# Kernel tuning notes

Hardware: AMD Instinct MI355X
Metric: run time of the kernel (lower is better)

Reference implementation:

```python
import jax, jax.numpy as jnp
import numpy as np

N_CHANNEL = 64
N_BAND = 5
N_CLASS = 2
B = 64
K = 2 * N_CHANNEL  # nodes covered by the fully-connected edge_index


def _w(key, shape):
    fan_in = shape[0] if len(shape) == 2 else int(np.prod(shape[1:]))
    return (jax.random.normal(key, shape, jnp.float32) / np.float32(np.sqrt(fan_in)))


def setup_inputs() -> dict:
    key = jax.random.key(0)
    ks = jax.random.split(key, 22)
    d = {}
    d['x1'] = jax.random.normal(ks[0], (B, K, N_BAND), jnp.float32)
    d['x2'] = jax.random.normal(ks[1], (B, K, K), jnp.float32)
    # GCNConv params (weights stored (in, out); PyG applies linear then aggregates, bias after)
    d['gcn1_w'] = _w(ks[2], (N_BAND, 2 * N_BAND))
    d['gcn1_b'] = 0.01 * jax.random.normal(ks[3], (2 * N_BAND,), jnp.float32)
    d['gcn2_w'] = _w(ks[4], (2 * N_BAND, 1))
    d['gcn2_b'] = 0.01 * jax.random.normal(ks[5], (1,), jnp.float32)
    d['fcg_w'] = _w(ks[6], (K, K))
    d['fcg_b'] = 0.01 * jax.random.normal(ks[7], (K,), jnp.float32)
    d['conv1_w'] = _w(ks[8], (16, 1, 3, 3))   # OIHW
    d['conv1_b'] = 0.01 * jax.random.normal(ks[9], (16,), jnp.float32)
    d['conv2_w'] = _w(ks[10], (16, 16, 3, 3))
    d['conv2_b'] = 0.01 * jax.random.normal(ks[11], (16,), jnp.float32)
    d['fcc_w'] = _w(ks[12], (16 * K * K, K))
    d['fcc_b'] = 0.01 * jax.random.normal(ks[13], (K,), jnp.float32)
    d['fc1_w'] = _w(ks[14], (4 * N_CHANNEL, 2 * N_CHANNEL))
    d['fc1_b'] = 0.01 * jax.random.normal(ks[15], (2 * N_CHANNEL,), jnp.float32)
    d['fc2_w'] = _w(ks[16], (2 * N_CHANNEL, N_CHANNEL))
    d['fc2_b'] = 0.01 * jax.random.normal(ks[17], (N_CHANNEL,), jnp.float32)
    d['fc3_w'] = _w(ks[18], (N_CHANNEL, N_CLASS))
    d['fc3_b'] = 0.01 * jax.random.normal(ks[19], (N_CLASS,), jnp.float32)
    return d


def _gcn(x, W, b):
    # Faithful to original: edge_index is fully connected over the FIRST K rows only.
    # With default self-loops, normalized adjacency over rows [0,K) is (1/K)*ones(K,K)
    # (all degrees = K); every other row has only its self-loop (degree 1 -> identity).
    y = x @ W                                   # (B*N, out)
    y = y.at[:K].set(jnp.mean(y[:K], axis=0))   # broadcast mean over first K rows
    return y + b


def _conv(x, w, b):
    y = jax.lax.conv_general_dilated(x, w, (1, 1), 'SAME',
                                     dimension_numbers=('NCHW', 'OIHW', 'NCHW'))
    return jax.nn.relu(y + b[None, :, None, None])


def reference(x1, x2, gcn1_w, gcn1_b, gcn2_w, gcn2_b, fcg_w, fcg_b,
              conv1_w, conv1_b, conv2_w, conv2_b, fcc_w, fcc_b,
              fc1_w, fc1_b, fc2_w, fc2_b, fc3_w, fc3_b):
    Bn, N, Feat = x1.shape
    # GNN branch (dropout is identity in eval mode)
    h = x1.reshape(Bn * N, Feat)
    h = jax.nn.relu(_gcn(h, gcn1_w, gcn1_b))
    h = jax.nn.relu(_gcn(h, gcn2_w, gcn2_b))
    h = h.reshape(Bn, -1)                       # (B, 2*n_channel)
    g = jax.nn.relu(h @ fcg_w + fcg_b)
    # CNN branch
    c = x2[:, None]                             # (B,1,H,W)
    c = _conv(c, conv1_w, conv1_b)
    c = _conv(c, conv2_w, conv2_b)
    c = c.reshape(Bn, -1)                       # channel-major flatten, same as torch .view
    c = jax.nn.relu(c @ fcc_w + fcc_b)
    # Fusion MLP
    x = jnp.concatenate([c, g], axis=1)
    x = jax.nn.relu(x @ fc1_w + fc1_b)
    x = jax.nn.relu(x @ fc2_w + fc2_b)
    return jax.nn.sigmoid(x @ fc3_w + fc3_b)
```

## Files before the change

### kernel.cpp

```cpp
#include <hip/hip_runtime.h>
#include <hip/hip_bf16.h>


#define NROWS   8192
#define IMG     16384
#define FCC_K   262144
#define FCC_BLOCKS 512
#define FCC_KRANGE 512
#define FCC_CHUNK 64
#define FCC_NCHUNK 8

typedef __attribute__((ext_vector_type(8))) short bf16x8;
typedef __attribute__((ext_vector_type(4))) float f32x4;
typedef __attribute__((ext_vector_type(4))) unsigned short us4;
typedef __attribute__((ext_vector_type(8))) unsigned short us8;

__device__ __forceinline__ unsigned short f2bf(float f) {
    unsigned u = __float_as_uint(f);
    unsigned r = (u + 0x7FFFu + ((u >> 16) & 1u)) >> 16;
    return (unsigned short)r;
}

__device__ __forceinline__ int fcc_swz64(int col, int k) {
    return col*64 + (k ^ ((((col >> 2) ^ col) & 7) << 3));
}

__global__ __launch_bounds__(256) void conv12_kernel(
    const float* __restrict__ x2,
    const float* __restrict__ w1,
    const float* __restrict__ b1,
    const float* __restrict__ w2,
    const float* __restrict__ b2,
    unsigned short* __restrict__ c2bf)
{
    __shared__ float sx2[8][130];
    __shared__ unsigned short sin[6*130*16];
    __shared__ unsigned short sB[5*512];
    __shared__ float sw1[144], sb1v[16];

    int tid = threadIdx.x;
    int blk = blockIdx.x;
    int b   = blk >> 5;
    int R0  = (blk & 31) * 4;

    if (tid < 144) sw1[tid] = w1[tid];
    if (tid < 16)  sb1v[tid] = b1[tid];

    for (int idx = tid; idx < 2560; idx += 256) {
        int q   = idx >> 9;
        int rem = idx & 511;
        int l   = rem >> 3;
        int e   = rem & 7;
        int k   = (l >> 4) * 8 + e;
        int oc  = l & 15;
        int ic  = k & 15;
        int dd  = 2*q + (k >> 4);
        unsigned short bits = 0;
        if (dd < 9) bits = f2bf(w2[oc*144 + ic*9 + dd]);
        sB[idx] = bits;
    }
    if (tid < 192) {
        int rr = tid >> 5, rem = tid & 31;
        int cc = (rem < 16) ? 0 : 129;
        sin[(rr*130 + cc)*16 + (rem & 15)] = 0;
    }
    {
        const float* xb = x2 + (size_t)b * IMG;
        for (int idx = tid; idx < 8*130; idx += 256) {
            int rr = idx / 130, cc = idx - rr*130;
            int ri = R0 - 2 + rr, gj = cc - 1;
            float v = 0.f;
            if (ri >= 0 && ri < 128 && gj >= 0 && gj < 128)
                v = xb[ri*128 + gj];
            sx2[rr][cc] = v;
        }
    }
    __syncthreads();

    for (int p = tid; p < 768; p += 256) {
        int rr = p >> 7;
        int cc = p & 127;
        int ri1 = R0 - 1 + rr;
        bool valid = (ri1 >= 0 && ri1 < 128);
        float in9[3][3];
        #pragma unroll
        for (int di = 0; di < 3; ++di)
          #pragma unroll
          for (int dj = 0; dj < 3; ++dj)
              in9[di][dj] = sx2[rr + di][cc + dj];
        us8 o0, o1;
        #pragma unroll
        for (int oc = 0; oc < 16; ++oc) {
            float acc = sb1v[oc];
            #pragma unroll
            for (int di = 0; di < 3; ++di)
              #pragma unroll
              for (int dj = 0; dj < 3; ++dj)
                  acc += in9[di][dj] * sw1[oc*9 + di*3 + dj];
            unsigned short bits = valid ? f2bf(fmaxf(acc, 0.f)) : (unsigned short)0;
            if (oc < 8) o0[oc] = bits; else o1[oc - 8] = bits;
        }
        unsigned short* dst = &sin[(rr*130 + cc + 1)*16];
        *reinterpret_cast<us8*>(dst)     = o0;
        *reinterpret_cast<us8*>(dst + 8) = o1;
    }
    __syncthreads();

    int lane = tid & 63;
    int wv   = tid >> 6;
    int ln   = lane & 15;
    int g    = lane >> 4;
    int ghalf = g & 1;

    int aoff[5];
    #pragma unroll
    for (int q = 0; q < 5; ++q) {
        int dd = 2*q + (g >> 1);
        if (dd > 8) dd = 8;
        int di = dd / 3, dj = dd % 3;
        aoff[q] = ((wv + di)*130 + ln + dj)*16 + ghalf*8;
    }

    bf16x8 bf[5];
    #pragma unroll
    for (int q = 0; q < 5; ++q)
        bf[q] = *reinterpret_cast<const bf16x8*>(&sB[q*512 + lane*8]);

    float bias_oc = b2[ln];
    int r = R0 + wv;
    unsigned short* outbase = c2bf + ((size_t)b*16 + ln)*IMG + r*128;

    #pragma unroll
    for (int t = 0; t < 8; ++t) {
        f32x4 acc = {0.f, 0.f, 0.f, 0.f};
        #pragma unroll
        for (int q = 0; q < 5; ++q) {
            bf16x8 a = *reinterpret_cast<const bf16x8*>(&sin[aoff[q] + t*256]);
            acc = __builtin_amdgcn_mfma_f32_16x16x32_bf16(a, bf[q], acc, 0, 0, 0);
        }
        int pc = t*16 + g*4;
        us4 pk;
        #pragma unroll
        for (int reg = 0; reg < 4; ++reg)
            pk[reg] = f2bf(fmaxf(acc[reg] + bias_oc, 0.f));
        *reinterpret_cast<us4*>(&outbase[pc]) = pk;
    }
}

__global__ __launch_bounds__(256, 2) void fcc_mfma(
    const unsigned short* __restrict__ c2bf,
    const float* __restrict__ W,
    float* __restrict__ partials)
{
    __shared__ unsigned short sWt[2][FCC_CHUNK*128];

    int tid  = threadIdx.x;
    int blk  = blockIdx.x;
    int k0   = blk * FCC_KRANGE;
    int lane = tid & 63, wv = tid >> 6;
    int ln   = lane & 15, g = lane >> 4;
    int q    = tid & 31;
    int kO   = tid >> 5;

    f32x4 acc[8];
    #pragma unroll
    for (int j = 0; j < 8; ++j) acc[j] = (f32x4){0.f,0.f,0.f,0.f};

    const float* Wb = W + (size_t)k0 * 128;
    const unsigned short* arow = c2bf + (size_t)(16*wv + ln)*FCC_K + k0 + g*8;
    int col0 = q*4;

    float4 rows[8];
    bf16x8 afc0, afc1, afn0, afn1;

    #pragma unroll
    for (int r = 0; r < 8; ++r)
        rows[r] = *reinterpret_cast<const float4*>(
            Wb + (size_t)(kO*8 + r)*128 + col0);
    afc0 = *reinterpret_cast<const bf16x8*>(arow);
    afc1 = *reinterpret_cast<const bf16x8*>(arow + 32);
    {
        us8 vc0, vc1, vc2, vc3;
        #pragma unroll
        for (int r = 0; r < 8; ++r) {
            vc0[r] = f2bf(rows[r].x); vc1[r] = f2bf(rows[r].y);
            vc2[r] = f2bf(rows[r].z); vc3[r] = f2bf(rows[r].w);
        }
        *reinterpret_cast<us8*>(&sWt[0][fcc_swz64(col0+0, kO*8)]) = vc0;
        *reinterpret_cast<us8*>(&sWt[0][fcc_swz64(col0+1, kO*8)]) = vc1;
        *reinterpret_cast<us8*>(&sWt[0][fcc_swz64(col0+2, kO*8)]) = vc2;
        *reinterpret_cast<us8*>(&sWt[0][fcc_swz64(col0+3, kO*8)]) = vc3;
    }
    __syncthreads();

    for (int ci = 0; ci < FCC_NCHUNK; ++ci) {
        const unsigned short* bufC = &sWt[ci & 1][0];
        if (ci < FCC_NCHUNK-1) {
            const float* Wc = Wb + (size_t)(ci + 1) * FCC_CHUNK * 128;
            #pragma unroll
            for (int r = 0; r < 8; ++r)
                rows[r] = *reinterpret_cast<const float4*>(
                    Wc + (size_t)(kO*8 + r)*128 + col0);
            afn0 = *reinterpret_cast<const bf16x8*>(arow + (ci+1)*FCC_CHUNK);
            afn1 = *reinterpret_cast<const bf16x8*>(arow + (ci+1)*FCC_CHUNK + 32);
        }
        #pragma unroll
        for (int j = 0; j < 8; ++j) {
            bf16x8 bfrag = *reinterpret_cast<const bf16x8*>(
                &bufC[fcc_swz64(j*16 + ln, g*8)]);
            acc[j] = __builtin_amdgcn_mfma_f32_16x16x32_bf16(afc0, bfrag, acc[j], 0, 0, 0);
        }
        #pragma unroll
        for (int j = 0; j < 8; ++j) {
            bf16x8 bfrag = *reinterpret_cast<const bf16x8*>(
                &bufC[fcc_swz64(j*16 + ln, 32 + g*8)]);
            acc[j] = __builtin_amdgcn_mfma_f32_16x16x32_bf16(afc1, bfrag, acc[j], 0, 0, 0);
        }
        __syncthreads();
        if (ci < FCC_NCHUNK-1) {
            unsigned short* bufN = &sWt[(ci + 1) & 1][0];
            us8 vc0, vc1, vc2, vc3;
            #pragma unroll
            for (int r = 0; r < 8; ++r) {
                vc0[r] = f2bf(rows[r].x); vc1[r] = f2bf(rows[r].y);
                vc2[r] = f2bf(rows[r].z); vc3[r] = f2bf(rows[r].w);
            }
            *reinterpret_cast<us8*>(&bufN[fcc_swz64(col0+0, kO*8)]) = vc0;
            *reinterpret_cast<us8*>(&bufN[fcc_swz64(col0+1, kO*8)]) = vc1;
            *reinterpret_cast<us8*>(&bufN[fcc_swz64(col0+2, kO*8)]) = vc2;
            *reinterpret_cast<us8*>(&bufN[fcc_swz64(col0+3, kO*8)]) = vc3;
            afc0 = afn0; afc1 = afn1;
        }
        __syncthreads();
    }

    float* p = partials + (size_t)blk * 8192;
    #pragma unroll
    for (int j = 0; j < 8; ++j)
      #pragma unroll
      for (int reg = 0; reg < 4; ++reg) {
          int m = 16*wv + g*4 + reg;
          p[m*128 + j*16 + ln] = acc[j][reg];
      }
}

__global__ __launch_bounds__(512) void head_kernel(
    const float* __restrict__ partials,
    const float* __restrict__ fccb,
    const float* __restrict__ x1,
    const float* __restrict__ gW1,
    const float* __restrict__ gb1,
    const float* __restrict__ gW2,
    const float* __restrict__ gb2,
    const float* __restrict__ fcgW,
    const float* __restrict__ fcgb,
    const float* __restrict__ w1, const float* __restrict__ bb1,
    const float* __restrict__ w2, const float* __restrict__ bb2,
    const float* __restrict__ w3, const float* __restrict__ bb3,
    float* __restrict__ out)
{
    __shared__ float sred[4][128];
    __shared__ float sx[256], sh[128], s2[64], sh2[128];
    __shared__ float sW1[50], sb1s[10], sW2s[10], smean[10];
    __shared__ float sy1[128][10];
    int b = blockIdx.x, t = threadIdx.x;
    int o = t & 127, pr = t >> 7;

    {
        const float* pb = partials + (size_t)pr*8192 + (size_t)b*128 + o;
        float s = 0.f;
        #pragma unroll 8
        for (int p = 0; p < FCC_BLOCKS/4; ++p) s += pb[(size_t)p*4*8192];
        sred[pr][o] = s;
    }
    if (t < 50) sW1[t] = gW1[t];
    if (t >= 64 && t < 74) { sb1s[t-64] = gb1[t-64]; sW2s[t-64] = gW2[t-64]; }
    __syncthreads();

    if (t < 128)
        sx[t] = fmaxf(sred[0][t] + sred[1][t] + sred[2][t] + sred[3][t]
                      + fccb[t], 0.f);

    float y[10];
    if (t < 128) {
        int r = b*128 + t;
        float x[5];
        #pragma unroll
        for (int f = 0; f < 5; ++f) x[f] = x1[r*5 + f];
        #pragma unroll
        for (int oo = 0; oo < 10; ++oo) {
            float a = 0.f;
            #pragma unroll
            for (int f = 0; f < 5; ++f) a += x[f] * sW1[f*10 + oo];
            y[oo] = a;
        }
    }
    if (b == 0) {
        if (t < 128) {
            #pragma unroll
            for (int oo = 0; oo < 10; ++oo) sy1[t][oo] = y[oo];
        }
        __syncthreads();
        if (t < 10) {
            float s = 0.f;
            for (int rr = 0; rr < 128; ++rr) s += sy1[rr][t];
            smean[t] = fmaxf(s * (1.f/128.f) + sb1s[t], 0.f);
        }
        __syncthreads();
    }
    if (t < 128) {
        float h1row[10];
        if (b == 0) {
            #pragma unroll
            for (int oo = 0; oo < 10; ++oo) h1row[oo] = smean[oo];
        } else {
            #pragma unroll
            for (int oo = 0; oo < 10; ++oo) h1row[oo] = fmaxf(y[oo] + sb1s[oo], 0.f);
        }
        float y2 = 0.f;
        #pragma unroll
        for (int oo = 0; oo < 10; ++oo) y2 += h1row[oo] * sW2s[oo];
        sh2[t] = fmaxf(y2 + gb2[0], 0.f);
    }
    __syncthreads();

    if (t < 128) {
        float acc = fcgb[t];
        #pragma unroll 8
        for (int k = 0; k < 128; ++k) acc += sh2[k] * fcgW[k*128 + t];
        sx[128 + t] = fmaxf(acc, 0.f);
    }
    __syncthreads();

    if (t < 128) {
        float acc = bb1[t];
        for (int k = 0; k < 256; ++k) acc += sx[k] * w1[k*128 + t];
        sh[t] = fmaxf(acc, 0.f);
    }
    __syncthreads();
    if (t < 64) {
        float acc = bb2[t];
        for (int k = 0; k < 128; ++k) acc += sh[k] * w2[k*64 + t];
        s2[t] = fmaxf(acc, 0.f);
    }
    __syncthreads();
    if (t < 2) {
        float acc = bb3[t];
        for (int k = 0; k < 64; ++k) acc += s2[k] * w3[k*2 + t];
        out[b*2 + t] = 1.f / (1.f + __expf(-acc));
    }
}

extern "C" void kernel_launch(void* const* d_in, const int* in_sizes, int n_in,
                              void* d_out, int out_size, void* d_ws, size_t ws_size,
                              hipStream_t stream)
{
    const float* x1      = (const float*)d_in[0];
    const float* x2      = (const float*)d_in[1];
    const float* gcn1_w  = (const float*)d_in[2];
    const float* gcn1_b  = (const float*)d_in[3];
    const float* gcn2_w  = (const float*)d_in[4];
    const float* gcn2_b  = (const float*)d_in[5];
    const float* fcg_w   = (const float*)d_in[6];
    const float* fcg_b   = (const float*)d_in[7];
    const float* conv1_w = (const float*)d_in[8];
    const float* conv1_b = (const float*)d_in[9];
    const float* conv2_w = (const float*)d_in[10];
    const float* conv2_b = (const float*)d_in[11];
    const float* fcc_w   = (const float*)d_in[12];
    const float* fcc_b   = (const float*)d_in[13];
    const float* fc1_w   = (const float*)d_in[14];
    const float* fc1_b   = (const float*)d_in[15];
    const float* fc2_w   = (const float*)d_in[16];
    const float* fc2_b   = (const float*)d_in[17];
    const float* fc3_w   = (const float*)d_in[18];
    const float* fc3_b   = (const float*)d_in[19];
    float* out = (float*)d_out;

    unsigned short* c2bf = (unsigned short*)d_ws;
    float* partials = (float*)(c2bf + 16777216);

    conv12_kernel<<<2048, 256, 0, stream>>>(x2, conv1_w, conv1_b,
                                            conv2_w, conv2_b, c2bf);
    fcc_mfma<<<FCC_BLOCKS, 256, 0, stream>>>(c2bf, fcc_w, partials);
    head_kernel<<<64, 512, 0, stream>>>(partials, fcc_b,
                                        x1, gcn1_w, gcn1_b, gcn2_w, gcn2_b,
                                        fcg_w, fcg_b,
                                        fc1_w, fc1_b, fc2_w, fc2_b,
                                        fc3_w, fc3_b, out);
}
```

Baseline: 90.25 us.

## Fuse conv, FC and head kernels into one persistent kernel with grid barriers

```diff
diff --git a/kernel.cpp b/kernel.cpp
--- a/kernel.cpp
+++ b/kernel.cpp
@@ -2,13 +2,13 @@
 #include <hip/hip_bf16.h>
 
 
-#define NROWS   8192
 #define IMG     16384
 #define FCC_K   262144
 #define FCC_BLOCKS 512
 #define FCC_KRANGE 512
 #define FCC_CHUNK 64
 #define FCC_NCHUNK 8
+#define GRID 512
 
 typedef __attribute__((ext_vector_type(8))) short bf16x8;
 typedef __attribute__((ext_vector_type(4))) float f32x4;
@@ -25,329 +25,358 @@
     return col*64 + (k ^ ((((col >> 2) ^ col) & 7) << 3));
 }
 
-__global__ __launch_bounds__(256) void conv12_kernel(
-    const float* __restrict__ x2,
-    const float* __restrict__ w1,
-    const float* __restrict__ b1,
-    const float* __restrict__ w2,
-    const float* __restrict__ b2,
-    unsigned short* __restrict__ c2bf)
-{
-    __shared__ float sx2[8][130];
-    __shared__ unsigned short sin[6*130*16];
-    __shared__ unsigned short sB[5*512];
-    __shared__ float sw1[144], sb1v[16];
-
-    int tid = threadIdx.x;
-    int blk = blockIdx.x;
-    int b   = blk >> 5;
-    int R0  = (blk & 31) * 4;
-
-    if (tid < 144) sw1[tid] = w1[tid];
-    if (tid < 16)  sb1v[tid] = b1[tid];
-
-    for (int idx = tid; idx < 2560; idx += 256) {
-        int q   = idx >> 9;
-        int rem = idx & 511;
-        int l   = rem >> 3;
-        int e   = rem & 7;
-        int k   = (l >> 4) * 8 + e;
-        int oc  = l & 15;
-        int ic  = k & 15;
-        int dd  = 2*q + (k >> 4);
-        unsigned short bits = 0;
-        if (dd < 9) bits = f2bf(w2[oc*144 + ic*9 + dd]);
-        sB[idx] = bits;
-    }
-    if (tid < 192) {
-        int rr = tid >> 5, rem = tid & 31;
-        int cc = (rem < 16) ? 0 : 129;
-        sin[(rr*130 + cc)*16 + (rem & 15)] = 0;
-    }
-    {
-        const float* xb = x2 + (size_t)b * IMG;
-        for (int idx = tid; idx < 8*130; idx += 256) {
-            int rr = idx / 130, cc = idx - rr*130;
-            int ri = R0 - 2 + rr, gj = cc - 1;
-            float v = 0.f;
-            if (ri >= 0 && ri < 128 && gj >= 0 && gj < 128)
-                v = xb[ri*128 + gj];
-            sx2[rr][cc] = v;
-        }
+__device__ __forceinline__ void grid_barrier(unsigned* bar, unsigned target) {
+    __syncthreads();
+    if (threadIdx.x == 0) {
+        __hip_atomic_fetch_add(bar, 1u, __ATOMIC_ACQ_REL, __HIP_MEMORY_SCOPE_AGENT);
+        while (__hip_atomic_load(bar, __ATOMIC_ACQUIRE, __HIP_MEMORY_SCOPE_AGENT) < target)
+            __builtin_amdgcn_s_sleep(2);
     }
     __syncthreads();
-
-    for (int p = tid; p < 768; p += 256) {
-        int rr = p >> 7;
-        int cc = p & 127;
-        int ri1 = R0 - 1 + rr;
-        bool valid = (ri1 >= 0 && ri1 < 128);
-        float in9[3][3];
-        #pragma unroll
-        for (int di = 0; di < 3; ++di)
-          #pragma unroll
-          for (int dj = 0; dj < 3; ++dj)
-              in9[di][dj] = sx2[rr + di][cc + dj];
-        us8 o0, o1;
-        #pragma unroll
-        for (int oc = 0; oc < 16; ++oc) {
-            float acc = sb1v[oc];
-            #pragma unroll
-            for (int di = 0; di < 3; ++di)
-              #pragma unroll
-              for (int dj = 0; dj < 3; ++dj)
-                  acc += in9[di][dj] * sw1[oc*9 + di*3 + dj];
-            unsigned short bits = valid ? f2bf(fmaxf(acc, 0.f)) : (unsigned short)0;
-            if (oc < 8) o0[oc] = bits; else o1[oc - 8] = bits;
-        }
-        unsigned short* dst = &sin[(rr*130 + cc + 1)*16];
-        *reinterpret_cast<us8*>(dst)     = o0;
-        *reinterpret_cast<us8*>(dst + 8) = o1;
-    }
-    __syncthreads();
-
-    int lane = tid & 63;
-    int wv   = tid >> 6;
-    int ln   = lane & 15;
-    int g    = lane >> 4;
-    int ghalf = g & 1;
-
-    int aoff[5];
-    #pragma unroll
-    for (int q = 0; q < 5; ++q) {
-        int dd = 2*q + (g >> 1);
-        if (dd > 8) dd = 8;
-        int di = dd / 3, dj = dd % 3;
-        aoff[q] = ((wv + di)*130 + ln + dj)*16 + ghalf*8;
-    }
-
-    bf16x8 bf[5];
-    #pragma unroll
-    for (int q = 0; q < 5; ++q)
-        bf[q] = *reinterpret_cast<const bf16x8*>(&sB[q*512 + lane*8]);
-
-    float bias_oc = b2[ln];
-    int r = R0 + wv;
-    unsigned short* outbase = c2bf + ((size_t)b*16 + ln)*IMG + r*128;
-
-    #pragma unroll
-    for (int t = 0; t < 8; ++t) {
-        f32x4 acc = {0.f, 0.f, 0.f, 0.f};
+}
+
+__global__ __launch_bounds__(256, 2) void mega_kernel(
+    const float* __restrict__ x1,
+    const float* __restrict__ x2,
+    const float* __restrict__ gW1, const float* __restrict__ gb1,
+    const float* __restrict__ gW2, const float* __restrict__ gb2,
+    const float* __restrict__ fcgW, const float* __restrict__ fcgb,
+    const float* __restrict__ w1c, const float* __restrict__ b1c,
+    const float* __restrict__ w2c, const float* __restrict__ b2c,
+    const float* __restrict__ fccW, const float* __restrict__ fccb,
+    const float* __restrict__ fw1, const float* __restrict__ fb1,
+    const float* __restrict__ fw2, const float* __restrict__ fb2,
+    const float* __restrict__ fw3, const float* __restrict__ fb3,
+    float* __restrict__ out,
+    unsigned short* __restrict__ c2bf,
+    float* __restrict__ partials,
+    float* __restrict__ cvec,
+    unsigned* __restrict__ bar)
+{
+    __shared__ __align__(16) unsigned char smem[35072];
+    int tid = threadIdx.x;
+    int cb  = blockIdx.x;
+
+    {
+        float* sx2           = (float*)smem;
+        unsigned short* sin_ = (unsigned short*)(smem + 4160);
+        unsigned short* sB   = (unsigned short*)(smem + 29120);
+        float* sw1           = (float*)(smem + 34240);
+        float* sb1v          = (float*)(smem + 34816);
+
+        if (tid < 144) sw1[tid] = w1c[tid];
+        if (tid < 16)  sb1v[tid] = b1c[tid];
+        for (int idx = tid; idx < 2560; idx += 256) {
+            int q   = idx >> 9;
+            int rem = idx & 511;
+            int l   = rem >> 3;
+            int e   = rem & 7;
+            int k   = (l >> 4) * 8 + e;
+            int oc  = l & 15;
+            int ic  = k & 15;
+            int dd  = 2*q + (k >> 4);
+            unsigned short bits = 0;
+            if (dd < 9) bits = f2bf(w2c[oc*144 + ic*9 + dd]);
+            sB[idx] = bits;
+        }
+        if (tid < 192) {
+            int rr = tid >> 5, rem = tid & 31;
+            int cc = (rem < 16) ? 0 : 129;
+            sin_[(rr*130 + cc)*16 + (rem & 15)] = 0;
+        }
+        __syncthreads();
+
+        int lane = tid & 63;
+        int wv   = tid >> 6;
+        int ln   = lane & 15;
+        int g    = lane >> 4;
+        int ghalf = g & 1;
+
+        int aoff[5];
         #pragma unroll
         for (int q = 0; q < 5; ++q) {
-            bf16x8 a = *reinterpret_cast<const bf16x8*>(&sin[aoff[q] + t*256]);
-            acc = __builtin_amdgcn_mfma_f32_16x16x32_bf16(a, bf[q], acc, 0, 0, 0);
-        }
-        int pc = t*16 + g*4;
-        us4 pk;
+            int dd = 2*q + (g >> 1);
+            if (dd > 8) dd = 8;
+            int di = dd / 3, dj = dd % 3;
+            aoff[q] = ((wv + di)*130 + ln + dj)*16 + ghalf*8;
+        }
+        bf16x8 bfr[5];
         #pragma unroll
-        for (int reg = 0; reg < 4; ++reg)
-            pk[reg] = f2bf(fmaxf(acc[reg] + bias_oc, 0.f));
-        *reinterpret_cast<us4*>(&outbase[pc]) = pk;
+        for (int q = 0; q < 5; ++q)
+            bfr[q] = *reinterpret_cast<const bf16x8*>(&sB[q*512 + lane*8]);
+        float bias_oc = b2c[ln];
+
+        for (int it = 0; it < 4; ++it) {
+            int blk = cb + GRID*it;
+            int b   = blk >> 5;
+            int R0  = (blk & 31) * 4;
+
+            {
+                const float* xb = x2 + (size_t)b * IMG;
+                for (int idx = tid; idx < 8*130; idx += 256) {
+                    int rr = idx / 130, cc = idx - rr*130;
+                    int ri = R0 - 2 + rr, gj = cc - 1;
+                    float v = 0.f;
+                    if (ri >= 0 && ri < 128 && gj >= 0 && gj < 128)
+                        v = xb[ri*128 + gj];
+                    sx2[rr*130 + cc] = v;
+                }
+            }
+            __syncthreads();
+
+            for (int p = tid; p < 768; p += 256) {
+                int rr = p >> 7;
+                int cc = p & 127;
+                int ri1 = R0 - 1 + rr;
+                bool valid = (ri1 >= 0 && ri1 < 128);
+                float in9[3][3];
+                #pragma unroll
+                for (int di = 0; di < 3; ++di)
+                  #pragma unroll
+                  for (int dj = 0; dj < 3; ++dj)
+                      in9[di][dj] = sx2[(rr + di)*130 + cc + dj];
+                us8 o0, o1;
+                #pragma unroll
+                for (int oc = 0; oc < 16; ++oc) {
+                    float acc = sb1v[oc];
+                    #pragma unroll
+                    for (int di = 0; di < 3; ++di)
+                      #pragma unroll
+                      for (int dj = 0; dj < 3; ++dj)
+                          acc += in9[di][dj] * sw1[oc*9 + di*3 + dj];
+                    unsigned short bits = valid ? f2bf(fmaxf(acc, 0.f))
+                                                : (unsigned short)0;
+                    if (oc < 8) o0[oc] = bits; else o1[oc - 8] = bits;
+                }
+                unsigned short* dst = &sin_[(rr*130 + cc + 1)*16];
+                *reinterpret_cast<us8*>(dst)     = o0;
+                *reinterpret_cast<us8*>(dst + 8) = o1;
+            }
+            __syncthreads();
+
+            int r = R0 + wv;
+            unsigned short* outbase = c2bf + ((size_t)b*16 + ln)*IMG + r*128;
+            #pragma unroll
+            for (int t8 = 0; t8 < 8; ++t8) {
+                f32x4 acc = {0.f, 0.f, 0.f, 0.f};
+                #pragma unroll
+                for (int q = 0; q < 5; ++q) {
+                    bf16x8 a = *reinterpret_cast<const bf16x8*>(
+                        &sin_[aoff[q] + t8*256]);
+                    acc = __builtin_amdgcn_mfma_f32_16x16x32_bf16(a, bfr[q], acc, 0, 0, 0);
+                }
+                int pc = t8*16 + g*4;
+                us4 pk;
+                #pragma unroll
+                for (int reg = 0; reg < 4; ++reg)
+                    pk[reg] = f2bf(fmaxf(acc[reg] + bias_oc, 0.f));
+                *reinterpret_cast<us4*>(&outbase[pc]) = pk;
+            }
+        }
     }
-}
-
-__global__ __launch_bounds__(256, 2) void fcc_mfma(
-    const unsigned short* __restrict__ c2bf,
-    const float* __restrict__ W,
-    float* __restrict__ partials)
-{
-    __shared__ unsigned short sWt[2][FCC_CHUNK*128];
-
-    int tid  = threadIdx.x;
-    int blk  = blockIdx.x;
-    int k0   = blk * FCC_KRANGE;
-    int lane = tid & 63, wv = tid >> 6;
-    int ln   = lane & 15, g = lane >> 4;
-    int q    = tid & 31;
-    int kO   = tid >> 5;
-
-    f32x4 acc[8];
-    #pragma unroll
-    for (int j = 0; j < 8; ++j) acc[j] = (f32x4){0.f,0.f,0.f,0.f};
-
-    const float* Wb = W + (size_t)k0 * 128;
-    const unsigned short* arow = c2bf + (size_t)(16*wv + ln)*FCC_K + k0 + g*8;
-    int col0 = q*4;
-
-    float4 rows[8];
-    bf16x8 afc0, afc1, afn0, afn1;
-
-    #pragma unroll
-    for (int r = 0; r < 8; ++r)
-        rows[r] = *reinterpret_cast<const float4*>(
-            Wb + (size_t)(kO*8 + r)*128 + col0);
-    afc0 = *reinterpret_cast<const bf16x8*>(arow);
-    afc1 = *reinterpret_cast<const bf16x8*>(arow + 32);
+
+    grid_barrier(bar, GRID);
+
     {
-        us8 vc0, vc1, vc2, vc3;
+        unsigned short* sWt = (unsigned short*)smem;
+        int blk  = cb;
+        int k0   = blk * FCC_KRANGE;
+        int lane = tid & 63, wv = tid >> 6;
+        int ln   = lane & 15, g = lane >> 4;
+        int q    = tid & 31;
+        int kO   = tid >> 5;
+
+        f32x4 acc[8];
         #pragma unroll
-        for (int r = 0; r < 8; ++r) {
-            vc0[r] = f2bf(rows[r].x); vc1[r] = f2bf(rows[r].y);
-            vc2[r] = f2bf(rows[r].z); vc3[r] = f2bf(rows[r].w);
-        }
-        *reinterpret_cast<us8*>(&sWt[0][fcc_swz64(col0+0, kO*8)]) = vc0;
-        *reinterpret_cast<us8*>(&sWt[0][fcc_swz64(col0+1, kO*8)]) = vc1;
-        *reinterpret_cast<us8*>(&sWt[0][fcc_swz64(col0+2, kO*8)]) = vc2;
-        *reinterpret_cast<us8*>(&sWt[0][fcc_swz64(col0+3, kO*8)]) = vc3;
-    }
-    __syncthreads();
-
-    for (int ci = 0; ci < FCC_NCHUNK; ++ci) {
-        const unsigned short* bufC = &sWt[ci & 1][0];
-        if (ci < FCC_NCHUNK-1) {
-            const float* Wc = Wb + (size_t)(ci + 1) * FCC_CHUNK * 128;
-            #pragma unroll
-            for (int r = 0; r < 8; ++r)
-                rows[r] = *reinterpret_cast<const float4*>(
-                    Wc + (size_t)(kO*8 + r)*128 + col0);
-            afn0 = *reinterpret_cast<const bf16x8*>(arow + (ci+1)*FCC_CHUNK);
-            afn1 = *reinterpret_cast<const bf16x8*>(arow + (ci+1)*FCC_CHUNK + 32);
-        }
+        for (int j = 0; j < 8; ++j) acc[j] = (f32x4){0.f,0.f,0.f,0.f};
+
+        const float* Wb = fccW + (size_t)k0 * 128;
+        const unsigned short* arow = c2bf + (size_t)(16*wv + ln)*FCC_K + k0 + g*8;
+        int col0 = q*4;
+
+        float4 rows[8];
+        bf16x8 afc0, afc1, afn0, afn1;
+
         #pragma unroll
-        for (int j = 0; j < 8; ++j) {
-            bf16x8 bfrag = *reinterpret_cast<const bf16x8*>(
-                &bufC[fcc_swz64(j*16 + ln, g*8)]);
-            acc[j] = __builtin_amdgcn_mfma_f32_16x16x32_bf16(afc0, bfrag, acc[j], 0, 0, 0);
-        }
-        #pragma unroll
-        for (int j = 0; j < 8; ++j) {
-            bf16x8 bfrag = *reinterpret_cast<const bf16x8*>(
-                &bufC[fcc_swz64(j*16 + ln, 32 + g*8)]);
-            acc[j] = __builtin_amdgcn_mfma_f32_16x16x32_bf16(afc1, bfrag, acc[j], 0, 0, 0);
-        }
-        __syncthreads();
-        if (ci < FCC_NCHUNK-1) {
-            unsigned short* bufN = &sWt[(ci + 1) & 1][0];
+        for (int r = 0; r < 8; ++r)
+            rows[r] = *reinterpret_cast<const float4*>(
+                Wb + (size_t)(kO*8 + r)*128 + col0);
+        afc0 = *reinterpret_cast<const bf16x8*>(arow);
+        afc1 = *reinterpret_cast<const bf16x8*>(arow + 32);
+        {
             us8 vc0, vc1, vc2, vc3;
             #pragma unroll
             for (int r = 0; r < 8; ++r) {
                 vc0[r] = f2bf(rows[r].x); vc1[r] = f2bf(rows[r].y);
                 vc2[r] = f2bf(rows[r].z); vc3[r] = f2bf(rows[r].w);
             }
-            *reinterpret_cast<us8*>(&bufN[fcc_swz64(col0+0, kO*8)]) = vc0;
-            *reinterpret_cast<us8*>(&bufN[fcc_swz64(col0+1, kO*8)]) = vc1;
-            *reinterpret_cast<us8*>(&bufN[fcc_swz64(col0+2, kO*8)]) = vc2;
-            *reinterpret_cast<us8*>(&bufN[fcc_swz64(col0+3, kO*8)]) = vc3;
-            afc0 = afn0; afc1 = afn1;
-        }
-        __syncthreads();
+            *reinterpret_cast<us8*>(&sWt[fcc_swz64(col0+0, kO*8)]) = vc0;
+            *reinterpret_cast<us8*>(&sWt[fcc_swz64(col0+1, kO*8)]) = vc1;
+            *reinterpret_cast<us8*>(&sWt[fcc_swz64(col0+2, kO*8)]) = vc2;
+            *reinterpret_cast<us8*>(&sWt[fcc_swz64(col0+3, kO*8)]) = vc3;
+        }
+        __syncthreads();
+
+        for (int ci = 0; ci < FCC_NCHUNK; ++ci) {
+            const unsigned short* bufC = &sWt[(ci & 1) * 8192];
+            if (ci < FCC_NCHUNK-1) {
+                const float* Wc = Wb + (size_t)(ci + 1) * FCC_CHUNK * 128;
+                #pragma unroll
+                for (int r = 0; r < 8; ++r)
+                    rows[r] = *reinterpret_cast<const float4*>(
+                        Wc + (size_t)(kO*8 + r)*128 + col0);
+                afn0 = *reinterpret_cast<const bf16x8*>(arow + (ci+1)*FCC_CHUNK);
+                afn1 = *reinterpret_cast<const bf16x8*>(arow + (ci+1)*FCC_CHUNK + 32);
+            }
+            #pragma unroll
+            for (int j = 0; j < 8; ++j) {
+                bf16x8 bfrag = *reinterpret_cast<const bf16x8*>(
+                    &bufC[fcc_swz64(j*16 + ln, g*8)]);
+                acc[j] = __builtin_amdgcn_mfma_f32_16x16x32_bf16(afc0, bfrag, acc[j], 0, 0, 0);
+            }
+            #pragma unroll
+            for (int j = 0; j < 8; ++j) {
+                bf16x8 bfrag = *reinterpret_cast<const bf16x8*>(
+                    &bufC[fcc_swz64(j*16 + ln, 32 + g*8)]);
+                acc[j] = __builtin_amdgcn_mfma_f32_16x16x32_bf16(afc1, bfrag, acc[j], 0, 0, 0);
+            }
+            __syncthreads();
+            if (ci < FCC_NCHUNK-1) {
+                unsigned short* bufN = &sWt[((ci + 1) & 1) * 8192];
+                us8 vc0, vc1, vc2, vc3;
+                #pragma unroll
+                for (int r = 0; r < 8; ++r) {
+                    vc0[r] = f2bf(rows[r].x); vc1[r] = f2bf(rows[r].y);
+                    vc2[r] = f2bf(rows[r].z); vc3[r] = f2bf(rows[r].w);
+                }
+                *reinterpret_cast<us8*>(&bufN[fcc_swz64(col0+0, kO*8)]) = vc0;
+                *reinterpret_cast<us8*>(&bufN[fcc_swz64(col0+1, kO*8)]) = vc1;
+                *reinterpret_cast<us8*>(&bufN[fcc_swz64(col0+2, kO*8)]) = vc2;
+                *reinterpret_cast<us8*>(&bufN[fcc_swz64(col0+3, kO*8)]) = vc3;
+                afc0 = afn0; afc1 = afn1;
+            }
+            __syncthreads();
+        }
+
+        float* p = partials + (size_t)blk * 8192;
+        #pragma unroll
+        for (int j = 0; j < 8; ++j)
+          #pragma unroll
+          for (int reg = 0; reg < 4; ++reg) {
+              int m = 16*wv + g*4 + reg;
+              p[m*128 + j*16 + ln] = acc[j][reg];
+          }
     }
 
-    float* p = partials + (size_t)blk * 8192;
-    #pragma unroll
-    for (int j = 0; j < 8; ++j)
-      #pragma unroll
-      for (int reg = 0; reg < 4; ++reg) {
-          int m = 16*wv + g*4 + reg;
-          p[m*128 + j*16 + ln] = acc[j][reg];
-      }
-}
-
-__global__ __launch_bounds__(512) void head_kernel(
-    const float* __restrict__ partials,
-    const float* __restrict__ fccb,
-    const float* __restrict__ x1,
-    const float* __restrict__ gW1,
-    const float* __restrict__ gb1,
-    const float* __restrict__ gW2,
-    const float* __restrict__ gb2,
-    const float* __restrict__ fcgW,
-    const float* __restrict__ fcgb,
-    const float* __restrict__ w1, const float* __restrict__ bb1,
-    const float* __restrict__ w2, const float* __restrict__ bb2,
-    const float* __restrict__ w3, const float* __restrict__ bb3,
-    float* __restrict__ out)
-{
-    __shared__ float sred[4][128];
-    __shared__ float sx[256], sh[128], s2[64], sh2[128];
-    __shared__ float sW1[50], sb1s[10], sW2s[10], smean[10];
-    __shared__ float sy1[128][10];
-    int b = blockIdx.x, t = threadIdx.x;
-    int o = t & 127, pr = t >> 7;
+    grid_barrier(bar, 2*GRID);
 
     {
-        const float* pb = partials + (size_t)pr*8192 + (size_t)b*128 + o;
+        float* sred = (float*)smem;
+        int O0 = cb*16;
+        int o  = tid & 15, pg = tid >> 4;
+        const float* pb = partials + (size_t)pg*8192 + O0 + o;
         float s = 0.f;
         #pragma unroll 8
-        for (int p = 0; p < FCC_BLOCKS/4; ++p) s += pb[(size_t)p*4*8192];
-        sred[pr][o] = s;
+        for (int i = 0; i < 32; ++i) s += pb[(size_t)i*16*8192];
+        sred[tid] = s;
+        __syncthreads();
+        if (tid < 16) {
+            float v = 0.f;
+            #pragma unroll
+            for (int p2 = 0; p2 < 16; ++p2) v += sred[p2*16 + tid];
+            int oo = O0 + tid;
+            cvec[oo] = fmaxf(v + fccb[oo & 127], 0.f);
+        }
     }
-    if (t < 50) sW1[t] = gW1[t];
-    if (t >= 64 && t < 74) { sb1s[t-64] = gb1[t-64]; sW2s[t-64] = gW2[t-64]; }
-    __syncthreads();
-
-    if (t < 128)
-        sx[t] = fmaxf(sred[0][t] + sred[1][t] + sred[2][t] + sred[3][t]
-                      + fccb[t], 0.f);
-
-    float y[10];
-    if (t < 128) {
-        int r = b*128 + t;
-        float x[5];
-        #pragma unroll
-        for (int f = 0; f < 5; ++f) x[f] = x1[r*5 + f];
-        #pragma unroll
-        for (int oo = 0; oo < 10; ++oo) {
-            float a = 0.f;
-            #pragma unroll
-            for (int f = 0; f < 5; ++f) a += x[f] * sW1[f*10 + oo];
-            y[oo] = a;
-        }
-    }
-    if (b == 0) {
+
+    grid_barrier(bar, 3*GRID);
+
+    if (cb < 64) {
+        float* fBm  = (float*)smem;
+        float* sx   = fBm;
+        float* sh   = fBm + 256;
+        float* s2   = fBm + 384;
+        float* sh2  = fBm + 448;
+        float* sW1  = fBm + 576;
+        float* sb1s = fBm + 626;
+        float* sW2s = fBm + 636;
+        float* smean= fBm + 646;
+        float* sy1  = fBm + 656;
+        int b = cb, t = tid;
+
+        if (t < 50) sW1[t] = gW1[t];
+        if (t >= 64 && t < 74) { sb1s[t-64] = gb1[t-64]; sW2s[t-64] = gW2[t-64]; }
+        if (t < 128) sx[t] = cvec[b*128 + t];
+        __syncthreads();
+
+        float y[10];
         if (t < 128) {
-            #pragma unroll
-            for (int oo = 0; oo < 10; ++oo) sy1[t][oo] = y[oo];
-        }
-        __syncthreads();
-        if (t < 10) {
-            float s = 0.f;
-            for (int rr = 0; rr < 128; ++rr) s += sy1[rr][t];
-            smean[t] = fmaxf(s * (1.f/128.f) + sb1s[t], 0.f);
-        }
-        __syncthreads();
-    }
-    if (t < 128) {
-        float h1row[10];
+            int r = b*128 + t;
+            float x[5];
+            #pragma unroll
+            for (int f = 0; f < 5; ++f) x[f] = x1[r*5 + f];
+            #pragma unroll
+            for (int oo = 0; oo < 10; ++oo) {
+                float a = 0.f;
+                #pragma unroll
+                for (int f = 0; f < 5; ++f) a += x[f] * sW1[f*10 + oo];
+                y[oo] = a;
+            }
+        }
         if (b == 0) {
-            #pragma unroll
-            for (int oo = 0; oo < 10; ++oo) h1row[oo] = smean[oo];
-        } else {
-            #pragma unroll
-            for (int oo = 0; oo < 10; ++oo) h1row[oo] = fmaxf(y[oo] + sb1s[oo], 0.f);
-        }
-        float y2 = 0.f;
-        #pragma unroll
-        for (int oo = 0; oo < 10; ++oo) y2 += h1row[oo] * sW2s[oo];
-        sh2[t] = fmaxf(y2 + gb2[0], 0.f);
-    }
-    __syncthreads();
-
-    if (t < 128) {
-        float acc = fcgb[t];
-        #pragma unroll 8
-        for (int k = 0; k < 128; ++k) acc += sh2[k] * fcgW[k*128 + t];
-        sx[128 + t] = fmaxf(acc, 0.f);
-    }
-    __syncthreads();
-
-    if (t < 128) {
-        float acc = bb1[t];
-        for (int k = 0; k < 256; ++k) acc += sx[k] * w1[k*128 + t];
-        sh[t] = fmaxf(acc, 0.f);
-    }
-    __syncthreads();
-    if (t < 64) {
-        float acc = bb2[t];
-        for (int k = 0; k < 128; ++k) acc += sh[k] * w2[k*64 + t];
-        s2[t] = fmaxf(acc, 0.f);
-    }
-    __syncthreads();
-    if (t < 2) {
-        float acc = bb3[t];
-        for (int k = 0; k < 64; ++k) acc += s2[k] * w3[k*2 + t];
-        out[b*2 + t] = 1.f / (1.f + __expf(-acc));
+            if (t < 128) {
+                #pragma unroll
+                for (int oo = 0; oo < 10; ++oo) sy1[t*10 + oo] = y[oo];
+            }
+            __syncthreads();
+            if (t < 10) {
+                float s = 0.f;
+                for (int rr = 0; rr < 128; ++rr) s += sy1[rr*10 + t];
+                smean[t] = fmaxf(s * (1.f/128.f) + sb1s[t], 0.f);
+            }
+            __syncthreads();
+        }
+        if (t < 128) {
+            float h1row[10];
+            if (b == 0) {
+                #pragma unroll
+                for (int oo = 0; oo < 10; ++oo) h1row[oo] = smean[oo];
+            } else {
+                #pragma unroll
+                for (int oo = 0; oo < 10; ++oo) h1row[oo] = fmaxf(y[oo] + sb1s[oo], 0.f);
+            }
+            float y2 = 0.f;
+            #pragma unroll
+            for (int oo = 0; oo < 10; ++oo) y2 += h1row[oo] * sW2s[oo];
+            sh2[t] = fmaxf(y2 + gb2[0], 0.f);
+        }
+        __syncthreads();
+
+        if (t < 128) {
+            float acc = fcgb[t];
+            #pragma unroll 8
+            for (int k = 0; k < 128; ++k) acc += sh2[k] * fcgW[k*128 + t];
+            sx[128 + t] = fmaxf(acc, 0.f);
+        }
+        __syncthreads();
+
+        if (t < 128) {
+            float acc = fb1[t];
+            for (int k = 0; k < 256; ++k) acc += sx[k] * fw1[k*128 + t];
+            sh[t] = fmaxf(acc, 0.f);
+        }
+        __syncthreads();
+        if (t < 64) {
+            float acc = fb2[t];
+            for (int k = 0; k < 128; ++k) acc += sh[k] * fw2[k*64 + t];
+            s2[t] = fmaxf(acc, 0.f);
+        }
+        __syncthreads();
+        if (t < 2) {
+            float acc = fb3[t];
+            for (int k = 0; k < 64; ++k) acc += s2[k] * fw3[k*2 + t];
+            out[b*2 + t] = 1.f / (1.f + __expf(-acc));
+        }
     }
 }
 
@@ -379,13 +408,13 @@
 
     unsigned short* c2bf = (unsigned short*)d_ws;
     float* partials = (float*)(c2bf + 16777216);
-
-    conv12_kernel<<<2048, 256, 0, stream>>>(x2, conv1_w, conv1_b,
-                                            conv2_w, conv2_b, c2bf);
-    fcc_mfma<<<FCC_BLOCKS, 256, 0, stream>>>(c2bf, fcc_w, partials);
-    head_kernel<<<64, 512, 0, stream>>>(partials, fcc_b,
-                                        x1, gcn1_w, gcn1_b, gcn2_w, gcn2_b,
-                                        fcg_w, fcg_b,
-                                        fc1_w, fc1_b, fc2_w, fc2_b,
-                                        fc3_w, fc3_b, out);
+    float* cvec     = partials + 4194304;
+    unsigned* bar   = (unsigned*)(cvec + 8192);
+
+    hipMemsetAsync(bar, 0, 64, stream);
+    mega_kernel<<<GRID, 256, 0, stream>>>(
+        x1, x2, gcn1_w, gcn1_b, gcn2_w, gcn2_b, fcg_w, fcg_b,
+        conv1_w, conv1_b, conv2_w, conv2_b, fcc_w, fcc_b,
+        fc1_w, fc1_b, fc2_w, fc2_b, fc3_w, fc3_b,
+        out, c2bf, partials, cvec, bar);
 }
```

New measurement: 235.5 us. 161% more time.

## Split FCC into more blocks with bf16 partials and a separate parallel reduce kernel

Applied to the files above, without the earlier changes.

```diff
diff --git a/kernel.cpp b/kernel.cpp
--- a/kernel.cpp
+++ b/kernel.cpp
@@ -2,13 +2,12 @@
 #include <hip/hip_bf16.h>
 
 
-#define NROWS   8192
 #define IMG     16384
 #define FCC_K   262144
-#define FCC_BLOCKS 512
-#define FCC_KRANGE 512
+#define FCC_BLOCKS 1024
+#define FCC_KRANGE 256
 #define FCC_CHUNK 64
-#define FCC_NCHUNK 8
+#define FCC_NCHUNK 4
 
 typedef __attribute__((ext_vector_type(8))) short bf16x8;
 typedef __attribute__((ext_vector_type(4))) float f32x4;
@@ -19,6 +18,10 @@
     unsigned u = __float_as_uint(f);
     unsigned r = (u + 0x7FFFu + ((u >> 16) & 1u)) >> 16;
     return (unsigned short)r;
+}
+__device__ __forceinline__ float bf2f(unsigned short b) {
+    unsigned u = ((unsigned)b) << 16;
+    return __uint_as_float(u);
 }
 
 __device__ __forceinline__ int fcc_swz64(int col, int k) {
@@ -147,12 +150,12 @@
     }
 }
 
-__global__ __launch_bounds__(256, 2) void fcc_mfma(
+__global__ __launch_bounds__(256, 4) void fcc_mfma(
     const unsigned short* __restrict__ c2bf,
     const float* __restrict__ W,
-    float* __restrict__ partials)
-{
-    __shared__ unsigned short sWt[2][FCC_CHUNK*128];
+    unsigned short* __restrict__ partials)
+{
+    __shared__ unsigned short sWt[FCC_CHUNK*128];
 
     int tid  = threadIdx.x;
     int blk  = blockIdx.x;
@@ -161,6 +164,7 @@
     int ln   = lane & 15, g = lane >> 4;
     int q    = tid & 31;
     int kO   = tid >> 5;
+    int col0 = q*4;
 
     f32x4 acc[8];
     #pragma unroll
@@ -168,121 +172,102 @@
 
     const float* Wb = W + (size_t)k0 * 128;
     const unsigned short* arow = c2bf + (size_t)(16*wv + ln)*FCC_K + k0 + g*8;
-    int col0 = q*4;
-
-    float4 rows[8];
-    bf16x8 afc0, afc1, afn0, afn1;
-
-    #pragma unroll
-    for (int r = 0; r < 8; ++r)
-        rows[r] = *reinterpret_cast<const float4*>(
-            Wb + (size_t)(kO*8 + r)*128 + col0);
-    afc0 = *reinterpret_cast<const bf16x8*>(arow);
-    afc1 = *reinterpret_cast<const bf16x8*>(arow + 32);
-    {
-        us8 vc0, vc1, vc2, vc3;
-        #pragma unroll
-        for (int r = 0; r < 8; ++r) {
-            vc0[r] = f2bf(rows[r].x); vc1[r] = f2bf(rows[r].y);
-            vc2[r] = f2bf(rows[r].z); vc3[r] = f2bf(rows[r].w);
-        }
-        *reinterpret_cast<us8*>(&sWt[0][fcc_swz64(col0+0, kO*8)]) = vc0;
-        *reinterpret_cast<us8*>(&sWt[0][fcc_swz64(col0+1, kO*8)]) = vc1;
-        *reinterpret_cast<us8*>(&sWt[0][fcc_swz64(col0+2, kO*8)]) = vc2;
-        *reinterpret_cast<us8*>(&sWt[0][fcc_swz64(col0+3, kO*8)]) = vc3;
-    }
-    __syncthreads();
 
     for (int ci = 0; ci < FCC_NCHUNK; ++ci) {
-        const unsigned short* bufC = &sWt[ci & 1][0];
-        if (ci < FCC_NCHUNK-1) {
-            const float* Wc = Wb + (size_t)(ci + 1) * FCC_CHUNK * 128;
-            #pragma unroll
-            for (int r = 0; r < 8; ++r)
-                rows[r] = *reinterpret_cast<const float4*>(
-                    Wc + (size_t)(kO*8 + r)*128 + col0);
-            afn0 = *reinterpret_cast<const bf16x8*>(arow + (ci+1)*FCC_CHUNK);
-            afn1 = *reinterpret_cast<const bf16x8*>(arow + (ci+1)*FCC_CHUNK + 32);
-        }
-        #pragma unroll
-        for (int j = 0; j < 8; ++j) {
-            bf16x8 bfrag = *reinterpret_cast<const bf16x8*>(
-                &bufC[fcc_swz64(j*16 + ln, g*8)]);
-            acc[j] = __builtin_amdgcn_mfma_f32_16x16x32_bf16(afc0, bfrag, acc[j], 0, 0, 0);
-        }
-        #pragma unroll
-        for (int j = 0; j < 8; ++j) {
-            bf16x8 bfrag = *reinterpret_cast<const bf16x8*>(
-                &bufC[fcc_swz64(j*16 + ln, 32 + g*8)]);
-            acc[j] = __builtin_amdgcn_mfma_f32_16x16x32_bf16(afc1, bfrag, acc[j], 0, 0, 0);
-        }
-        __syncthreads();
-        if (ci < FCC_NCHUNK-1) {
-            unsigned short* bufN = &sWt[(ci + 1) & 1][0];
+        const float* Wc = Wb + (size_t)ci * FCC_CHUNK * 128;
+        float4 rows[8];
+        #pragma unroll
+        for (int r = 0; r < 8; ++r)
+            rows[r] = *reinterpret_cast<const float4*>(
+                Wc + (size_t)(kO*8 + r)*128 + col0);
+        {
             us8 vc0, vc1, vc2, vc3;
             #pragma unroll
             for (int r = 0; r < 8; ++r) {
                 vc0[r] = f2bf(rows[r].x); vc1[r] = f2bf(rows[r].y);
                 vc2[r] = f2bf(rows[r].z); vc3[r] = f2bf(rows[r].w);
             }
-            *reinterpret_cast<us8*>(&bufN[fcc_swz64(col0+0, kO*8)]) = vc0;
-            *reinterpret_cast<us8*>(&bufN[fcc_swz64(col0+1, kO*8)]) = vc1;
-            *reinterpret_cast<us8*>(&bufN[fcc_swz64(col0+2, kO*8)]) = vc2;
-            *reinterpret_cast<us8*>(&bufN[fcc_swz64(col0+3, kO*8)]) = vc3;
-            afc0 = afn0; afc1 = afn1;
+            *reinterpret_cast<us8*>(&sWt[fcc_swz64(col0+0, kO*8)]) = vc0;
+            *reinterpret_cast<us8*>(&sWt[fcc_swz64(col0+1, kO*8)]) = vc1;
+            *reinterpret_cast<us8*>(&sWt[fcc_swz64(col0+2, kO*8)]) = vc2;
+            *reinterpret_cast<us8*>(&sWt[fcc_swz64(col0+3, kO*8)]) = vc3;
         }
         __syncthreads();
-    }
-
-    float* p = partials + (size_t)blk * 8192;
+
+        bf16x8 af0 = *reinterpret_cast<const bf16x8*>(arow + ci*FCC_CHUNK);
+        bf16x8 af1 = *reinterpret_cast<const bf16x8*>(arow + ci*FCC_CHUNK + 32);
+        #pragma unroll
+        for (int j = 0; j < 8; ++j) {
+            bf16x8 bfrag = *reinterpret_cast<const bf16x8*>(
+                &sWt[fcc_swz64(j*16 + ln, g*8)]);
+            acc[j] = __builtin_amdgcn_mfma_f32_16x16x32_bf16(af0, bfrag, acc[j], 0, 0, 0);
+        }
+        #pragma unroll
+        for (int j = 0; j < 8; ++j) {
+            bf16x8 bfrag = *reinterpret_cast<const bf16x8*>(
+                &sWt[fcc_swz64(j*16 + ln, 32 + g*8)]);
+            acc[j] = __builtin_amdgcn_mfma_f32_16x16x32_bf16(af1, bfrag, acc[j], 0, 0, 0);
+        }
+        __syncthreads();
+    }
+
+    unsigned short* p = partials + (size_t)blk * 8192;
     #pragma unroll
     for (int j = 0; j < 8; ++j)
       #pragma unroll
       for (int reg = 0; reg < 4; ++reg) {
           int m = 16*wv + g*4 + reg;
-          p[m*128 + j*16 + ln] = acc[j][reg];
+          p[m*128 + j*16 + ln] = f2bf(acc[j][reg]);
       }
 }
 
-__global__ __launch_bounds__(512) void head_kernel(
-    const float* __restrict__ partials,
-    const float* __restrict__ fccb,
+__global__ __launch_bounds__(256) void fcc_reduce(
+    const unsigned short* __restrict__ partials,
+    const float* __restrict__ bias,
+    float* __restrict__ cvec)
+{
+    __shared__ float sred[8][32];
+    int blk = blockIdx.x, t = threadIdx.x;
+    int o  = blk*32 + (t & 31);
+    int pr = t >> 5;
+    const unsigned short* pb = partials + (size_t)pr*8192 + o;
+    float s = 0.f;
+    #pragma unroll 16
+    for (int i = 0; i < FCC_BLOCKS/8; ++i)
+        s += bf2f(pb[(size_t)i*8*8192]);
+    sred[pr][t & 31] = s;
+    __syncthreads();
+    if (t < 32) {
+        float v = 0.f;
+        #pragma unroll
+        for (int p2 = 0; p2 < 8; ++p2) v += sred[p2][t];
+        cvec[o] = fmaxf(v + bias[o & 127], 0.f);
+    }
+}
+
+__global__ __launch_bounds__(128) void head_kernel(
+    const float* __restrict__ cvec,
     const float* __restrict__ x1,
-    const float* __restrict__ gW1,
-    const float* __restrict__ gb1,
-    const float* __restrict__ gW2,
-    const float* __restrict__ gb2,
-    const float* __restrict__ fcgW,
-    const float* __restrict__ fcgb,
+    const float* __restrict__ gW1, const float* __restrict__ gb1,
+    const float* __restrict__ gW2, const float* __restrict__ gb2,
+    const float* __restrict__ fcgW, const float* __restrict__ fcgb,
     const float* __restrict__ w1, const float* __restrict__ bb1,
     const float* __restrict__ w2, const float* __restrict__ bb2,
     const float* __restrict__ w3, const float* __restrict__ bb3,
     float* __restrict__ out)
 {
-    __shared__ float sred[4][128];
     __shared__ float sx[256], sh[128], s2[64], sh2[128];
     __shared__ float sW1[50], sb1s[10], sW2s[10], smean[10];
     __shared__ float sy1[128][10];
     int b = blockIdx.x, t = threadIdx.x;
-    int o = t & 127, pr = t >> 7;
-
-    {
-        const float* pb = partials + (size_t)pr*8192 + (size_t)b*128 + o;
-        float s = 0.f;
-        #pragma unroll 8
-        for (int p = 0; p < FCC_BLOCKS/4; ++p) s += pb[(size_t)p*4*8192];
-        sred[pr][o] = s;
-    }
+
     if (t < 50) sW1[t] = gW1[t];
     if (t >= 64 && t < 74) { sb1s[t-64] = gb1[t-64]; sW2s[t-64] = gW2[t-64]; }
-    __syncthreads();
-
-    if (t < 128)
-        sx[t] = fmaxf(sred[0][t] + sred[1][t] + sred[2][t] + sred[3][t]
-                      + fccb[t], 0.f);
+    sx[t] = cvec[b*128 + t];
+    __syncthreads();
 
     float y[10];
-    if (t < 128) {
+    {
         int r = b*128 + t;
         float x[5];
         #pragma unroll
@@ -296,10 +281,8 @@
         }
     }
     if (b == 0) {
-        if (t < 128) {
-            #pragma unroll
-            for (int oo = 0; oo < 10; ++oo) sy1[t][oo] = y[oo];
-        }
+        #pragma unroll
+        for (int oo = 0; oo < 10; ++oo) sy1[t][oo] = y[oo];
         __syncthreads();
         if (t < 10) {
             float s = 0.f;
@@ -308,7 +291,7 @@
         }
         __syncthreads();
     }
-    if (t < 128) {
+    {
         float h1row[10];
         if (b == 0) {
             #pragma unroll
@@ -324,7 +307,7 @@
     }
     __syncthreads();
 
-    if (t < 128) {
+    {
         float acc = fcgb[t];
         #pragma unroll 8
         for (int k = 0; k < 128; ++k) acc += sh2[k] * fcgW[k*128 + t];
@@ -332,7 +315,7 @@
     }
     __syncthreads();
 
-    if (t < 128) {
+    {
         float acc = bb1[t];
         for (int k = 0; k < 256; ++k) acc += sx[k] * w1[k*128 + t];
         sh[t] = fmaxf(acc, 0.f);
@@ -377,15 +360,16 @@
     const float* fc3_b   = (const float*)d_in[19];
     float* out = (float*)d_out;
 
-    unsigned short* c2bf = (unsigned short*)d_ws;
-    float* partials = (float*)(c2bf + 16777216);
+    unsigned short* c2bf     = (unsigned short*)d_ws;
+    unsigned short* partials = c2bf + 16777216;
+    float* cvec = (float*)(partials + 8388608);
 
     conv12_kernel<<<2048, 256, 0, stream>>>(x2, conv1_w, conv1_b,
                                             conv2_w, conv2_b, c2bf);
     fcc_mfma<<<FCC_BLOCKS, 256, 0, stream>>>(c2bf, fcc_w, partials);
-    head_kernel<<<64, 512, 0, stream>>>(partials, fcc_b,
-                                        x1, gcn1_w, gcn1_b, gcn2_w, gcn2_b,
-                                        fcg_w, fcg_b,
+    fcc_reduce<<<256, 256, 0, stream>>>(partials, fcc_b, cvec);
+    head_kernel<<<64, 128, 0, stream>>>(cvec, x1, gcn1_w, gcn1_b,
+                                        gcn2_w, gcn2_b, fcg_w, fcg_b,
                                         fc1_w, fc1_b, fc2_w, fc2_b,
                                         fc3_w, fc3_b, out);
 }
```

After: 96.49 us. 1.07x slower.
